# Kernel tuning notes

Measured on AMD Instinct MI355X. Metric: run time of the kernel, lower is better.

Reference implementation:

```python
import jax, jax.numpy as jnp
import numpy as np
import math

B, I, H = 8192, 1024, 1024


def setup_inputs() -> dict:
    key = jax.random.key(0)
    ks = jax.random.split(key, 16)
    stdv = 1.0 / math.sqrt(H)
    u = lambda k, shape: jax.random.uniform(k, shape, jnp.float32, -stdv, stdv)
    inp = {
        'xt': jax.random.normal(ks[0], (B, I), jnp.float32),
        'cx': jax.random.normal(ks[1], (B, H), jnp.float32),
        'hx': jax.random.normal(ks[2], (B, H), jnp.float32),
        'w_fg': u(ks[3], (H, I)), 'w_ig': u(ks[4], (H, I)),
        'w_og': u(ks[5], (H, I)), 'w_ci': u(ks[6], (H, I)),
        'r_fg': u(ks[7], (H, H)), 'r_ig': u(ks[8], (H, H)),
        'r_og': u(ks[9], (H, H)), 'r_ci': u(ks[10], (H, H)),
        'b_fg': u(ks[11], (H,)), 'b_ig': u(ks[12], (H,)),
        'b_og': u(ks[13], (H,)), 'b_ci': u(ks[14], (H,)),
    }
    return inp


def reference(xt, cx, hx, w_fg, w_ig, w_og, w_ci, r_fg, r_ig, r_og, r_ci,
              b_fg, b_ig, b_og, b_ci):
    # Fuse the four input matmuls and four recurrent matmuls into two GEMMs.
    W = jnp.concatenate([w_fg, w_ig, w_og, w_ci], axis=0)  # [4H, I]
    R = jnp.concatenate([r_fg, r_ig, r_og, r_ci], axis=0)  # [4H, H]
    b = jnp.concatenate([b_fg, b_ig, b_og, b_ci], axis=0)  # [4H]
    gates = xt @ W.T + hx @ R.T + b                         # [B, 4H]
    f, i, o, g = jnp.split(gates, 4, axis=-1)
    ft = jax.nn.sigmoid(f)
    it = jax.nn.sigmoid(i)
    ot = jax.nn.sigmoid(o)
    ct = ft * cx + it * jnp.tanh(g)
    ht = ot * jnp.tanh(ct)
    return (ht, ct)
```

## Files before the change

kernel.cpp:

```cpp
#include <hip/hip_runtime.h>

#define B_DIM 8192
#define H_DIM 1024
#define K_DIM 2048
#define N_DIM 4096
#define BH (B_DIM * H_DIM)
#define NT 32
#define TSZ (256 * 64)
#define HALFT (128 * 64)

using frag_ab = __attribute__((ext_vector_type(8))) short;
using frag_cd = __attribute__((ext_vector_type(4))) float;

__device__ __forceinline__ unsigned short f2bf(float f) {
  union { float f; unsigned u; } x; x.f = f;
  return (unsigned short)((x.u + 0x7fffu + ((x.u >> 16) & 1u)) >> 16);
}

__global__ __launch_bounds__(256) void convert_A_kernel(
    const float* __restrict__ xt, const float* __restrict__ hx,
    unsigned short* __restrict__ Ab) {
  int tid = blockIdx.x * 256 + threadIdx.x;
  int flat = tid * 4;
  int m = flat >> 11;
  int k = flat & 2047;
  const float* src = (k < 1024) ? (xt + m * 1024 + k)
                                : (hx + m * 1024 + (k - 1024));
  float4 v = *reinterpret_cast<const float4*>(src);
  ushort4 o;
  o.x = f2bf(v.x); o.y = f2bf(v.y); o.z = f2bf(v.z); o.w = f2bf(v.w);
  *reinterpret_cast<ushort4*>(Ab + flat) = o;
}

__global__ __launch_bounds__(256) void convert_B_kernel(
    const float* __restrict__ w0, const float* __restrict__ w1,
    const float* __restrict__ w2, const float* __restrict__ w3,
    const float* __restrict__ r0, const float* __restrict__ r1,
    const float* __restrict__ r2, const float* __restrict__ r3,
    unsigned short* __restrict__ Bb) {
  int tid = blockIdx.x * 256 + threadIdx.x;
  int flat = tid * 4;
  int n = flat >> 11;
  int k = flat & 2047;
  int tile = n >> 8, c = n & 255;
  int gate = (c >> 4) & 3;
  int h = tile * 64 + ((c >> 6) << 4) + (c & 15);
  const float* wb = (gate == 0) ? w0 : (gate == 1) ? w1 : (gate == 2) ? w2 : w3;
  const float* rb = (gate == 0) ? r0 : (gate == 1) ? r1 : (gate == 2) ? r2 : r3;
  const float* src = (k < 1024) ? (wb + h * 1024 + k)
                                : (rb + h * 1024 + (k - 1024));
  float4 v = *reinterpret_cast<const float4*>(src);
  ushort4 o;
  o.x = f2bf(v.x); o.y = f2bf(v.y); o.z = f2bf(v.z); o.w = f2bf(v.w);
  *reinterpret_cast<ushort4*>(Bb + flat) = o;
}

__device__ __forceinline__ void gload_lds16(const void* g, void* l) {
  __builtin_amdgcn_global_load_lds(
      (const __attribute__((address_space(1))) unsigned int*)g,
      (__attribute__((address_space(3))) unsigned int*)l, 16, 0, 0);
}

__device__ __forceinline__ frag_ab ldsr(const unsigned short* buf, int byteoff) {
  return *reinterpret_cast<const frag_ab*>(
      reinterpret_cast<const char*>(buf) + byteoff);
}

__device__ __forceinline__ float fast_sigmoid(float x) {
  return 1.f / (1.f + __expf(-x));
}
__device__ __forceinline__ float fast_tanh(float x) {
  return 1.f - 2.f / (__expf(2.f * x) + 1.f);
}

#define CBAR asm volatile("" ::: "memory")
#define SBAR do { CBAR; __builtin_amdgcn_s_barrier(); CBAR; } while (0)

#define TILE_BODY(Ac, Bc, Anx, Bnx, tt, S1, S2, S3, S4, DO_VM2, DO_VM0)        \
  {                                                                            \
                              \
    _Pragma("unroll") for (int m = 0; m < 4; ++m)                              \
        Af0[m] = ldsr(Ac, (arow + m * 16) * 128 + c0);                         \
    _Pragma("unroll") for (int n = 0; n < 4; ++n)                              \
        Bf0[n] = ldsr(Bc, (brow + n * 16) * 128 + c0);                         \
    if (S1) stage(Bg + 128 * K_DIM + (size_t)((tt) + 1) * 64, (Bnx) + HALFT);  \
    SBAR;                                                                      \
    __builtin_amdgcn_s_setprio(1);                                             \
    _Pragma("unroll") for (int m = 0; m < 4; ++m)                              \
        _Pragma("unroll") for (int n = 0; n < 4; ++n)                          \
            acc[m][n] = __builtin_amdgcn_mfma_f32_16x16x32_bf16(               \
                Af0[m], Bf0[n], acc[m][n], 0, 0, 0);                           \
    __builtin_amdgcn_s_setprio(0);                                             \
                              \
    _Pragma("unroll") for (int m = 0; m < 4; ++m)                              \
        Af1[m] = ldsr(Ac, (arow + m * 16) * 128 + c1);                         \
    _Pragma("unroll") for (int n = 0; n < 4; ++n)                              \
        Bf1[n] = ldsr(Bc, (brow + n * 16) * 128 + c1);                         \
    if (S2) stage(Ag + (size_t)((tt) + 1) * 64, (Anx));                        \
    SBAR;                                                                      \
    __builtin_amdgcn_s_setprio(1);                                             \
    _Pragma("unroll") for (int m = 0; m < 4; ++m)                              \
        _Pragma("unroll") for (int n = 0; n < 4; ++n)                          \
            acc[m][n] = __builtin_amdgcn_mfma_f32_16x16x32_bf16(               \
                Af1[m], Bf1[n], acc[m][n], 0, 0, 0);                           \
    __builtin_amdgcn_s_setprio(0);                                             \
                   \
    _Pragma("unroll") for (int m = 0; m < 4; ++m)                              \
        Af0[m] = ldsr(Ac, (arow + 64 + m * 16) * 128 + c0);                    \
    if (S3) stage(Ag + 128 * K_DIM + (size_t)((tt) + 1) * 64, (Anx) + HALFT);  \
    SBAR;                                                                      \
    __builtin_amdgcn_s_setprio(1);                                             \
    _Pragma("unroll") for (int m = 0; m < 4; ++m)                              \
        _Pragma("unroll") for (int n = 0; n < 4; ++n)                          \
            acc[4 + m][n] = __builtin_amdgcn_mfma_f32_16x16x32_bf16(           \
                Af0[m], Bf0[n], acc[4 + m][n], 0, 0, 0);                       \
    __builtin_amdgcn_s_setprio(0);                                             \
                   \
    _Pragma("unroll") for (int m = 0; m < 4; ++m)                              \
        Af1[m] = ldsr(Ac, (arow + 64 + m * 16) * 128 + c1);                    \
    if (S4) stage(Bg + (size_t)((tt) + 2) * 64, (Bc));                        \
    SBAR;                                                                      \
    __builtin_amdgcn_s_setprio(1);                                             \
    _Pragma("unroll") for (int m = 0; m < 4; ++m)                              \
        _Pragma("unroll") for (int n = 0; n < 4; ++n)                          \
            acc[4 + m][n] = __builtin_amdgcn_mfma_f32_16x16x32_bf16(           \
                Af1[m], Bf1[n], acc[4 + m][n], 0, 0, 0);                       \
    __builtin_amdgcn_s_setprio(0);                                             \
    if (DO_VM2) asm volatile("s_waitcnt vmcnt(2)" ::: "memory");               \
    if (DO_VM0) asm volatile("s_waitcnt vmcnt(0)" ::: "memory");               \
  }

__global__ __launch_bounds__(512, 2) void lstm_gemm_kernel(
    const unsigned short* __restrict__ Ab,
    const unsigned short* __restrict__ Bb,
    const float* __restrict__ cx,
    const float* __restrict__ b_f, const float* __restrict__ b_i,
    const float* __restrict__ b_o, const float* __restrict__ b_g,
    float* __restrict__ out) {
  extern __shared__ unsigned short smem[];
  unsigned short* const As0 = smem;
  unsigned short* const As1 = smem + TSZ;
  unsigned short* const Bs0 = smem + 2 * TSZ;
  unsigned short* const Bs1 = smem + 3 * TSZ;

  const int bid = blockIdx.x;
  const int swz = (bid & 7) * 64 + (bid >> 3);
  const int bm = swz >> 4;
  const int bn = swz & 15;

  const int tid = threadIdx.x;
  const int lane = tid & 63;
  const int wid = tid >> 6;
  const int wr = wid >> 2, wc = wid & 3;
  const int ln = lane & 15, kh = lane >> 4;

  const unsigned short* Ag = Ab + (size_t)(bm * 256) * K_DIM;
  const unsigned short* Bg = Bb + (size_t)(bn * 256) * K_DIM;

  const int srow = wid * 16 + (lane >> 3);
  const size_t gs0 = (size_t)srow * K_DIM + (((lane & 7) ^ (lane >> 3)) << 3);
  const size_t gs1 = gs0 + (size_t)8 * K_DIM;
  const int ld0 = wid * 2048 + lane * 16;
  const int ld1 = ld0 + 1024;
  auto stage = [&](const unsigned short* g, unsigned short* l) {
    gload_lds16(g + gs0, reinterpret_cast<char*>(l) + ld0);
    gload_lds16(g + gs1, reinterpret_cast<char*>(l) + ld1);
  };

  const int inv = (ln & 7) << 4;
  const int c0 = (kh * 16) ^ inv;
  const int c1 = (64 + kh * 16) ^ inv;
  const int arow = wr * 128 + ln;
  const int brow = wc * 64 + ln;

  frag_cd acc[8][4] = {};
  frag_ab Af0[4], Af1[4], Bf0[4], Bf1[4];

  stage(Ag, As0);
  stage(Ag + 128 * K_DIM, As0 + HALFT);
  stage(Bg, Bs0);
  stage(Bg + 128 * K_DIM, Bs0 + HALFT);
  stage(Bg + 64, Bs1);
  asm volatile("s_waitcnt vmcnt(2)" ::: "memory");
  SBAR;

  for (int u = 0; u < 15; ++u) {
    const int e = 2 * u;
    TILE_BODY(As0, Bs0, As1, Bs1, e, 1, 1, 1, 1, 1, 0);
    TILE_BODY(As1, Bs1, As0, Bs0, e + 1, 1, 1, 1, 1, 1, 0);
  }
  TILE_BODY(As0, Bs0, As1, Bs1, 30, 1, 1, 1, 0, 0, 1);
  TILE_BODY(As1, Bs1, As0, Bs0, 31, 0, 0, 0, 0, 0, 0);

  const int hcol = bn * 64 + wc * 16 + ln;
  const float bfv = b_f[hcol], biv = b_i[hcol], bov = b_o[hcol], bgv = b_g[hcol];
  const int row_base = bm * 256 + wr * 128 + kh * 4;
#pragma unroll
  for (int mi = 0; mi < 8; ++mi) {
#pragma unroll
    for (int j = 0; j < 4; ++j) {
      const int row = row_base + mi * 16 + j;
      float fp = acc[mi][0][j] + bfv;
      float ip = acc[mi][1][j] + biv;
      float op = acc[mi][2][j] + bov;
      float gp = acc[mi][3][j] + bgv;
      float ft = fast_sigmoid(fp);
      float it = fast_sigmoid(ip);
      float ot = fast_sigmoid(op);
      float gt = fast_tanh(gp);
      float cold = cx[(size_t)row * H_DIM + hcol];
      float ct = ft * cold + it * gt;
      float ht = ot * fast_tanh(ct);
      out[(size_t)row * H_DIM + hcol] = ht;
      out[BH + (size_t)row * H_DIM + hcol] = ct;
    }
  }
}

extern "C" void kernel_launch(void* const* d_in, const int* in_sizes, int n_in,
                              void* d_out, int out_size, void* d_ws, size_t ws_size,
                              hipStream_t stream) {
  const float* xt   = (const float*)d_in[0];
  const float* cxp  = (const float*)d_in[1];
  const float* hx   = (const float*)d_in[2];
  const float* w_fg = (const float*)d_in[3];
  const float* w_ig = (const float*)d_in[4];
  const float* w_og = (const float*)d_in[5];
  const float* w_ci = (const float*)d_in[6];
  const float* r_fg = (const float*)d_in[7];
  const float* r_ig = (const float*)d_in[8];
  const float* r_og = (const float*)d_in[9];
  const float* r_ci = (const float*)d_in[10];
  const float* b_fg = (const float*)d_in[11];
  const float* b_ig = (const float*)d_in[12];
  const float* b_og = (const float*)d_in[13];
  const float* b_ci = (const float*)d_in[14];

  unsigned short* Abf = (unsigned short*)d_ws;
  unsigned short* Bbf = Abf + (size_t)B_DIM * K_DIM;
  float* out = (float*)d_out;

  convert_A_kernel<<<dim3(B_DIM * K_DIM / 4 / 256), dim3(256), 0, stream>>>(
      xt, hx, Abf);
  convert_B_kernel<<<dim3(N_DIM * K_DIM / 4 / 256), dim3(256), 0, stream>>>(
      w_fg, w_ig, w_og, w_ci, r_fg, r_ig, r_og, r_ci, Bbf);
  lstm_gemm_kernel<<<dim3((B_DIM / 256) * (N_DIM / 256)), dim3(512),
                     131072, stream>>>(
      Abf, Bbf, cxp, b_fg, b_ig, b_og, b_ci, out);
}
```

Baseline: 154.6 us.

## Replace staggered four-barrier tile pipeline with simple double-buffer single barrier

The K-loop schedule changes. Previously each tile issued one prefetch stage and one barrier per quarter, with the B buffer prefetched two tiles ahead. Now all four prefetch stages for the next tile are issued at the top, followed by the four compute quarters with no barriers, a full vmcnt(0) wait and one barrier per tile. This removes three barriers per tile but gives up the finer interleaving and the deeper prefetch, so memory latency may be exposed at the end of each tile.

```diff
diff --git a/kernel.cpp b/kernel.cpp
--- a/kernel.cpp
+++ b/kernel.cpp
@@ -76,58 +76,56 @@
 #define CBAR asm volatile("" ::: "memory")
 #define SBAR do { CBAR; __builtin_amdgcn_s_barrier(); CBAR; } while (0)
 
-#define TILE_BODY(Ac, Bc, Anx, Bnx, tt, S1, S2, S3, S4, DO_VM2, DO_VM0)        \
+#define TILE_BODY(Ac, Bc, An, Bn, tt, S, ENDBAR)                               \
   {                                                                            \
-                              \
+    if (S) {                                                                   \
+      stage(Ag + (size_t)((tt) + 1) * 64, (An));                               \
+      stage(Ag + (size_t)((tt) + 1) * 64 + 128 * K_DIM, (An) + HALFT);         \
+      stage(Bg + (size_t)((tt) + 1) * 64, (Bn));                               \
+      stage(Bg + (size_t)((tt) + 1) * 64 + 128 * K_DIM, (Bn) + HALFT);         \
+    }                                                                          \
+                           \
     _Pragma("unroll") for (int m = 0; m < 4; ++m)                              \
         Af0[m] = ldsr(Ac, (arow + m * 16) * 128 + c0);                         \
     _Pragma("unroll") for (int n = 0; n < 4; ++n)                              \
         Bf0[n] = ldsr(Bc, (brow + n * 16) * 128 + c0);                         \
-    if (S1) stage(Bg + 128 * K_DIM + (size_t)((tt) + 1) * 64, (Bnx) + HALFT);  \
-    SBAR;                                                                      \
     __builtin_amdgcn_s_setprio(1);                                             \
     _Pragma("unroll") for (int m = 0; m < 4; ++m)                              \
         _Pragma("unroll") for (int n = 0; n < 4; ++n)                          \
             acc[m][n] = __builtin_amdgcn_mfma_f32_16x16x32_bf16(               \
                 Af0[m], Bf0[n], acc[m][n], 0, 0, 0);                           \
     __builtin_amdgcn_s_setprio(0);                                             \
-                              \
+                           \
     _Pragma("unroll") for (int m = 0; m < 4; ++m)                              \
         Af1[m] = ldsr(Ac, (arow + m * 16) * 128 + c1);                         \
     _Pragma("unroll") for (int n = 0; n < 4; ++n)                              \
         Bf1[n] = ldsr(Bc, (brow + n * 16) * 128 + c1);                         \
-    if (S2) stage(Ag + (size_t)((tt) + 1) * 64, (Anx));                        \
-    SBAR;                                                                      \
     __builtin_amdgcn_s_setprio(1);                                             \
     _Pragma("unroll") for (int m = 0; m < 4; ++m)                              \
         _Pragma("unroll") for (int n = 0; n < 4; ++n)                          \
             acc[m][n] = __builtin_amdgcn_mfma_f32_16x16x32_bf16(               \
                 Af1[m], Bf1[n], acc[m][n], 0, 0, 0);                           \
     __builtin_amdgcn_s_setprio(0);                                             \
-                   \
+                          \
     _Pragma("unroll") for (int m = 0; m < 4; ++m)                              \
         Af0[m] = ldsr(Ac, (arow + 64 + m * 16) * 128 + c0);                    \
-    if (S3) stage(Ag + 128 * K_DIM + (size_t)((tt) + 1) * 64, (Anx) + HALFT);  \
-    SBAR;                                                                      \
     __builtin_amdgcn_s_setprio(1);                                             \
     _Pragma("unroll") for (int m = 0; m < 4; ++m)                              \
         _Pragma("unroll") for (int n = 0; n < 4; ++n)                          \
             acc[4 + m][n] = __builtin_amdgcn_mfma_f32_16x16x32_bf16(           \
                 Af0[m], Bf0[n], acc[4 + m][n], 0, 0, 0);                       \
     __builtin_amdgcn_s_setprio(0);                                             \
-                   \
+                          \
     _Pragma("unroll") for (int m = 0; m < 4; ++m)                              \
         Af1[m] = ldsr(Ac, (arow + 64 + m * 16) * 128 + c1);                    \
-    if (S4) stage(Bg + (size_t)((tt) + 2) * 64, (Bc));                        \
-    SBAR;                                                                      \
     __builtin_amdgcn_s_setprio(1);                                             \
     _Pragma("unroll") for (int m = 0; m < 4; ++m)                              \
         _Pragma("unroll") for (int n = 0; n < 4; ++n)                          \
             acc[4 + m][n] = __builtin_amdgcn_mfma_f32_16x16x32_bf16(           \
                 Af1[m], Bf1[n], acc[4 + m][n], 0, 0, 0);                       \
     __builtin_amdgcn_s_setprio(0);                                             \
-    if (DO_VM2) asm volatile("s_waitcnt vmcnt(2)" ::: "memory");               \
-    if (DO_VM0) asm volatile("s_waitcnt vmcnt(0)" ::: "memory");               \
+    if (S) asm volatile("s_waitcnt vmcnt(0)" ::: "memory");                    \
+    if (ENDBAR) SBAR;                                                          \
   }
 
 __global__ __launch_bounds__(512, 2) void lstm_gemm_kernel(
@@ -157,8 +155,8 @@
   const unsigned short* Ag = Ab + (size_t)(bm * 256) * K_DIM;
   const unsigned short* Bg = Bb + (size_t)(bn * 256) * K_DIM;
 
-  const int srow = wid * 16 + (lane >> 3);
-  const size_t gs0 = (size_t)srow * K_DIM + (((lane & 7) ^ (lane >> 3)) << 3);
+  const size_t gs0 = (size_t)(wid * 16 + (lane >> 3)) * K_DIM +
+                     (((lane & 7) ^ (lane >> 3)) << 3);
   const size_t gs1 = gs0 + (size_t)8 * K_DIM;
   const int ld0 = wid * 2048 + lane * 16;
   const int ld1 = ld0 + 1024;
@@ -180,17 +178,16 @@
   stage(Ag + 128 * K_DIM, As0 + HALFT);
   stage(Bg, Bs0);
   stage(Bg + 128 * K_DIM, Bs0 + HALFT);
-  stage(Bg + 64, Bs1);
-  asm volatile("s_waitcnt vmcnt(2)" ::: "memory");
+  asm volatile("s_waitcnt vmcnt(0)" ::: "memory");
   SBAR;
 
   for (int u = 0; u < 15; ++u) {
     const int e = 2 * u;
-    TILE_BODY(As0, Bs0, As1, Bs1, e, 1, 1, 1, 1, 1, 0);
-    TILE_BODY(As1, Bs1, As0, Bs0, e + 1, 1, 1, 1, 1, 1, 0);
+    TILE_BODY(As0, Bs0, As1, Bs1, e, 1, 1);
+    TILE_BODY(As1, Bs1, As0, Bs0, e + 1, 1, 1);
   }
-  TILE_BODY(As0, Bs0, As1, Bs1, 30, 1, 1, 1, 0, 0, 1);
-  TILE_BODY(As1, Bs1, As0, Bs0, 31, 0, 0, 0, 0, 0, 0);
+  TILE_BODY(As0, Bs0, As1, Bs1, 30, 1, 1);
+  TILE_BODY(As1, Bs1, As0, Bs0, 31, 0, 0);
 
   const int hcol = bn * 64 + wc * 16 + ln;
   const float bfv = b_f[hcol], biv = b_i[hcol], bov = b_o[hcol], bgv = b_g[hcol];
```

Result: slower. 159.5 us (+3.2%).
